# Optimization experiments

Hardware: AMD Instinct MI355X
Metric: run time of the kernel (lower is better)

Reference implementation:

```python
import jax, jax.numpy as jnp
import numpy as np

F = 50  # number of feature fields

def setup_inputs() -> dict:
    key = jax.random.key(0)
    k1, k2, k3, k4 = jax.random.split(key, 4)
    B, D, A = 4096, 16, 32
    return {
        "feat_emb": jax.random.normal(k1, (B, F, D), dtype=jnp.float32),
        "W": jax.random.normal(k2, (D, A), dtype=jnp.float32) * 0.1,
        "h": jax.random.normal(k3, (A,), dtype=jnp.float32),
        "p_vec": jax.random.normal(k4, (D,), dtype=jnp.float32),
    }

def reference(feat_emb, W, h, p_vec):
    # build_cross: upper-triangular field pairs (i < j)
    row, col = np.triu_indices(F, k=1)              # each [P], P = F*(F-1)/2
    p = feat_emb[:, row]                             # [B, P, D]
    q = feat_emb[:, col]                             # [B, P, D]
    inter = p * q                                    # pairwise interaction [B, P, D]
    # AttLayer: Dense(no bias) -> relu -> contract with h -> softmax over pairs
    att_signal = jax.nn.relu(jnp.einsum('bpd,da->bpa', inter, W))  # [B, P, A]
    scores = jnp.einsum('bpa,a->bp', att_signal, h)                # [B, P]
    att = jax.nn.softmax(scores, axis=1)                           # [B, P]
    # attention-weighted sum-pooling over pairs
    pooled = jnp.einsum('bp,bpd->bd', att, inter)                  # [B, D]
    # dropout omitted (inference); final projection and reduce
    out = jnp.einsum('bd,d->b', pooled, p_vec)[:, None]            # [B, 1]
    return out
```

## Files before the change

### kernel.cpp

```cpp
#include <hip/hip_runtime.h>
#include <math.h>


#define FF 50
#define DD 16
#define AA 32
#define NP 1225
#define NT 39
#define NQ4 10
#define ERS 24
#define EBS (FF * ERS)
#define BPB 8
#define NTHR 512

typedef _Float16 half8 __attribute__((ext_vector_type(8)));
typedef _Float16 half4 __attribute__((ext_vector_type(4)));
typedef _Float16 half2v __attribute__((ext_vector_type(2)));
typedef __fp16   fh2    __attribute__((ext_vector_type(2)));
typedef float    floatx16 __attribute__((ext_vector_type(16)));

__global__ __launch_bounds__(NTHR, 4) void afm_kernel(
    const float* __restrict__ feat,
    const float* __restrict__ W,
    const float* __restrict__ h,
    const float* __restrict__ pvec,
    float* __restrict__ out,
    int Btot)
{
  __shared__ __align__(16) _Float16 eh[BPB * EBS];
  __shared__ __align__(16) unsigned int tbl[NQ4 * 128];

  const int tid    = threadIdx.x;
  const int lane   = tid & 63;
  const int wave   = tid >> 6;
  const int halfid = lane >> 5;
  const int n      = lane & 31;
  const int b0     = blockIdx.x * BPB;

  for (int s = tid; s < BPB * 200; s += NTHR) {
    int bl  = s / 200;
    int rem = s - bl * 200;
    int bb  = b0 + bl;
    if (bb < Btot) {
      float4 v4 = ((const float4*)feat)[(size_t)bb * 200 + rem];
      half4 hv;
      hv[0] = (_Float16)v4.x; hv[1] = (_Float16)v4.y;
      hv[2] = (_Float16)v4.z; hv[3] = (_Float16)v4.w;
      int row = rem >> 2, q = rem & 3;
      *(half4*)(&eh[bl * EBS + row * ERS + q * 4]) = hv;
    }
  }

  for (int q = tid; q < NQ4 * 128; q += NTHR) {
    int q4  = q >> 7;
    int rem = q & 127;
    int nn  = rem >> 2;
    int u   = rem & 3;
    int p   = (4 * q4 + u) * 32 + nn;
    unsigned ent = 0;
    if (p < NP) {
      int rad = 9801 - 8 * p;
      int i = (int)((99.0f - sqrtf((float)rad)) * 0.5f);
      if (i < 0) i = 0; if (i > 48) i = 48;
      int off = (i * (99 - i)) >> 1;
      if (off > p) { --i; off = (i * (99 - i)) >> 1; }
      else {
        int off1 = ((i + 1) * (98 - i)) >> 1;
        if (off1 <= p) { ++i; off = off1; }
      }
      int j = p - off + i + 1;
      ent = ((unsigned)(i * 48) << 16) | (unsigned)(j * 48);
    }
    tbl[q] = ent;
  }

  const float LOG2E = 1.4426950408889634f;
  half8 A0;
  #pragma unroll
  for (int jj = 0; jj < 8; ++jj)
    A0[jj] = (_Float16)W[(halfid * 8 + jj) * AA + n];
  fh2 h2[8];
  #pragma unroll
  for (int q = 0; q < 8; ++q) {
    h2[q][0] = (__fp16)(h[((2*q) & 3) + 8 * ((2*q) >> 2) + 4 * halfid] * LOG2E);
    h2[q][1] = (__fp16)(h[((2*q+1) & 3) + 8 * ((2*q+1) >> 2) + 4 * halfid] * LOG2E);
  }
  fh2 pv2[4];
  #pragma unroll
  for (int q = 0; q < 4; ++q) {
    pv2[q][0] = (__fp16)pvec[halfid * 8 + 2 * q];
    pv2[q][1] = (__fp16)pvec[halfid * 8 + 2 * q + 1];
  }
  const floatx16 ZACC = (floatx16)0.0f;
  const fh2 zz = {(__fp16)0.f, (__fp16)0.f};

  __syncthreads();

  const char* eb = (const char*)(eh + wave * EBS) + halfid * 16;
  const unsigned int* tq = tbl + n * 4;

#if __has_builtin(__builtin_amdgcn_exp2f)
  #define EXP2(x) __builtin_amdgcn_exp2f(x)
#else
  #define EXP2(x) exp2f(x)
#endif

  auto mkB = [&](unsigned ij, float& gout) -> half8 {
    half8 Bi = *(const half8*)(eb + (ij >> 16));
    half8 Bj = *(const half8*)(eb + (ij & 0xffffu));
    half8 Bv = Bi * Bj;
#if __has_builtin(__builtin_amdgcn_fdot2)
    fh2 q0 = __builtin_bit_cast(fh2, (half2v)__builtin_shufflevector(Bv, Bv, 0, 1));
    fh2 q1 = __builtin_bit_cast(fh2, (half2v)__builtin_shufflevector(Bv, Bv, 2, 3));
    fh2 q2 = __builtin_bit_cast(fh2, (half2v)__builtin_shufflevector(Bv, Bv, 4, 5));
    fh2 q3 = __builtin_bit_cast(fh2, (half2v)__builtin_shufflevector(Bv, Bv, 6, 7));
    gout = __builtin_amdgcn_fdot2(q1, pv2[1],
           __builtin_amdgcn_fdot2(q0, pv2[0], 0.f, false), false)
         + __builtin_amdgcn_fdot2(q3, pv2[3],
           __builtin_amdgcn_fdot2(q2, pv2[2], 0.f, false), false);
#else
    float gp = 0.f;
    #pragma unroll
    for (int k = 0; k < 8; ++k)
      gp = fmaf((float)Bv[k], (float)((const __fp16*)pv2)[k], gp);
    gout = gp;
#endif
    return Bv;
  };
  auto epi = [&](const floatx16& z) -> float {
    float vL = 0.f, vH = 0.f;
    #pragma unroll
    for (int q = 0; q < 4; ++q) {
      fh2 zp = __builtin_amdgcn_cvt_pkrtz(z[2*q], z[2*q+1]);
      fh2 zr = __builtin_elementwise_max(zp, zz);
      vL = __builtin_amdgcn_fdot2(zr, h2[q], vL, false);
    }
    #pragma unroll
    for (int q = 4; q < 8; ++q) {
      fh2 zp = __builtin_amdgcn_cvt_pkrtz(z[2*q], z[2*q+1]);
      fh2 zr = __builtin_elementwise_max(zp, zz);
      vH = __builtin_amdgcn_fdot2(zr, h2[q], vH, false);
    }
    return vL + vH;
  };

  float den0 = 0.f, num0 = 0.f, den1 = 0.f, num1 = 0.f;

  for (int q4 = 0; q4 < 9; ++q4) {
    uint4 cur = *(const uint4*)(tq + (q4 << 7));
    float g0, g1, g2, g3;
    half8 B0 = mkB(cur.x, g0);
    half8 B1 = mkB(cur.y, g1);
    half8 B2 = mkB(cur.z, g2);
    half8 B3 = mkB(cur.w, g3);
    floatx16 z0 = __builtin_amdgcn_mfma_f32_32x32x16_f16(A0, B0, ZACC, 0, 0, 0);
    floatx16 z1 = __builtin_amdgcn_mfma_f32_32x32x16_f16(A0, B1, ZACC, 0, 0, 0);
    floatx16 z2 = __builtin_amdgcn_mfma_f32_32x32x16_f16(A0, B2, ZACC, 0, 0, 0);
    floatx16 z3 = __builtin_amdgcn_mfma_f32_32x32x16_f16(A0, B3, ZACC, 0, 0, 0);
    float p0 = epi(z0), p1 = epi(z1), p2 = epi(z2), p3 = epi(z3);
    float s0 = __shfl_xor(p0, 32, 64);
    float s1 = __shfl_xor(p1, 32, 64);
    float s2 = __shfl_xor(p2, 32, 64);
    float s3 = __shfl_xor(p3, 32, 64);
    float ex0 = EXP2(p0 + s0), ex1 = EXP2(p1 + s1);
    float ex2 = EXP2(p2 + s2), ex3 = EXP2(p3 + s3);
    den0 += ex0; num0 = fmaf(ex0, g0, num0);
    den1 += ex1; num1 = fmaf(ex1, g1, num1);
    den0 += ex2; num0 = fmaf(ex2, g2, num0);
    den1 += ex3; num1 = fmaf(ex3, g3, num1);
  }
  {
    uint4 cur = *(const uint4*)(tq + (9 << 7));
    float g0, g1, g2;
    half8 B0 = mkB(cur.x, g0);
    half8 B1 = mkB(cur.y, g1);
    half8 B2 = mkB(cur.z, g2);
    floatx16 z0 = __builtin_amdgcn_mfma_f32_32x32x16_f16(A0, B0, ZACC, 0, 0, 0);
    floatx16 z1 = __builtin_amdgcn_mfma_f32_32x32x16_f16(A0, B1, ZACC, 0, 0, 0);
    floatx16 z2 = __builtin_amdgcn_mfma_f32_32x32x16_f16(A0, B2, ZACC, 0, 0, 0);
    float p0 = epi(z0), p1 = epi(z1), p2 = epi(z2);
    float s0 = __shfl_xor(p0, 32, 64);
    float s1 = __shfl_xor(p1, 32, 64);
    float s2 = __shfl_xor(p2, 32, 64);
    float v2 = (n < 9) ? (p2 + s2) : -3.0e38f;
    float ex0 = EXP2(p0 + s0), ex1 = EXP2(p1 + s1), ex2 = EXP2(v2);
    den0 += ex0; num0 = fmaf(ex0, g0, num0);
    den1 += ex1; num1 = fmaf(ex1, g1, num1);
    den0 += ex2; num0 = fmaf(ex2, g2, num0);
  }
  float den = den0 + den1, num = num0 + num1;

  #pragma unroll
  for (int mask = 32; mask >= 1; mask >>= 1) {
    den += __shfl_xor(den, mask, 64);
    num += __shfl_xor(num, mask, 64);
  }
  const int b = b0 + wave;
  if (lane == 0 && b < Btot) out[b] = (2.0f * num) / den;
}

extern "C" void kernel_launch(void* const* d_in, const int* in_sizes, int n_in,
                              void* d_out, int out_size, void* d_ws, size_t ws_size,
                              hipStream_t stream) {
  const float* feat = (const float*)d_in[0];
  const float* W    = (const float*)d_in[1];
  const float* h    = (const float*)d_in[2];
  const float* pvec = (const float*)d_in[3];
  float* out = (float*)d_out;
  const int B = in_sizes[0] / (FF * DD);
  afm_kernel<<<(B + BPB - 1) / BPB, NTHR, 0, stream>>>(feat, W, h, pvec, out, B);
}
```

Baseline: 81.45 us.

## Move score and projection dot products from fdot2 into MFMA instructions

Replaces the per-lane fdot2 reductions for the attention score (h contraction) and the p_vec projection with extra MFMA instructions. The relu'd accumulator fragments are repacked as B operands and multiplied by h-filled and p_vec-filled A matrices. This removes the cross-half shuffles and the dot-product VALU work. The cost is three extra MFMAs per tile, where only one output row of each is used, so matrix-core throughput is largely wasted.

```diff
diff --git a/kernel.cpp b/kernel.cpp
--- a/kernel.cpp
+++ b/kernel.cpp
@@ -15,9 +15,9 @@
 
 typedef _Float16 half8 __attribute__((ext_vector_type(8)));
 typedef _Float16 half4 __attribute__((ext_vector_type(4)));
-typedef _Float16 half2v __attribute__((ext_vector_type(2)));
 typedef __fp16   fh2    __attribute__((ext_vector_type(2)));
 typedef float    floatx16 __attribute__((ext_vector_type(16)));
+typedef unsigned int uintv4 __attribute__((ext_vector_type(4)));
 
 __global__ __launch_bounds__(NTHR, 4) void afm_kernel(
     const float* __restrict__ feat,
@@ -79,17 +79,13 @@
   #pragma unroll
   for (int jj = 0; jj < 8; ++jj)
     A0[jj] = (_Float16)W[(halfid * 8 + jj) * AA + n];
-  fh2 h2[8];
+  half8 A2_0, A2_16, Apv;
   #pragma unroll
-  for (int q = 0; q < 8; ++q) {
-    h2[q][0] = (__fp16)(h[((2*q) & 3) + 8 * ((2*q) >> 2) + 4 * halfid] * LOG2E);
-    h2[q][1] = (__fp16)(h[((2*q+1) & 3) + 8 * ((2*q+1) >> 2) + 4 * halfid] * LOG2E);
-  }
-  fh2 pv2[4];
-  #pragma unroll
-  for (int q = 0; q < 4; ++q) {
-    pv2[q][0] = (__fp16)pvec[halfid * 8 + 2 * q];
-    pv2[q][1] = (__fp16)pvec[halfid * 8 + 2 * q + 1];
+  for (int jj = 0; jj < 8; ++jj) {
+    int arow = 4 * halfid + (jj & 3) + 8 * (jj >> 2);
+    A2_0[jj]  = (_Float16)(h[arow]      * LOG2E);
+    A2_16[jj] = (_Float16)(h[16 + arow] * LOG2E);
+    Apv[jj]   = (_Float16)pvec[halfid * 8 + jj];
   }
   const floatx16 ZACC = (floatx16)0.0f;
   const fh2 zz = {(__fp16)0.f, (__fp16)0.f};
@@ -105,88 +101,67 @@
   #define EXP2(x) exp2f(x)
 #endif
 
-  auto mkB = [&](unsigned ij, float& gout) -> half8 {
+  auto mkB = [&](unsigned ij) -> half8 {
     half8 Bi = *(const half8*)(eb + (ij >> 16));
     half8 Bj = *(const half8*)(eb + (ij & 0xffffu));
-    half8 Bv = Bi * Bj;
-#if __has_builtin(__builtin_amdgcn_fdot2)
-    fh2 q0 = __builtin_bit_cast(fh2, (half2v)__builtin_shufflevector(Bv, Bv, 0, 1));
-    fh2 q1 = __builtin_bit_cast(fh2, (half2v)__builtin_shufflevector(Bv, Bv, 2, 3));
-    fh2 q2 = __builtin_bit_cast(fh2, (half2v)__builtin_shufflevector(Bv, Bv, 4, 5));
-    fh2 q3 = __builtin_bit_cast(fh2, (half2v)__builtin_shufflevector(Bv, Bv, 6, 7));
-    gout = __builtin_amdgcn_fdot2(q1, pv2[1],
-           __builtin_amdgcn_fdot2(q0, pv2[0], 0.f, false), false)
-         + __builtin_amdgcn_fdot2(q3, pv2[3],
-           __builtin_amdgcn_fdot2(q2, pv2[2], 0.f, false), false);
-#else
-    float gp = 0.f;
+    return Bi * Bj;
+  };
+
+  auto score_frags = [&](const floatx16& z, half8& BL, half8& BH) {
+    unsigned q[8];
     #pragma unroll
-    for (int k = 0; k < 8; ++k)
-      gp = fmaf((float)Bv[k], (float)((const __fp16*)pv2)[k], gp);
-    gout = gp;
-#endif
-    return Bv;
-  };
-  auto epi = [&](const floatx16& z) -> float {
-    float vL = 0.f, vH = 0.f;
-    #pragma unroll
-    for (int q = 0; q < 4; ++q) {
-      fh2 zp = __builtin_amdgcn_cvt_pkrtz(z[2*q], z[2*q+1]);
+    for (int i = 0; i < 8; ++i) {
+      fh2 zp = __builtin_amdgcn_cvt_pkrtz(z[2 * i], z[2 * i + 1]);
       fh2 zr = __builtin_elementwise_max(zp, zz);
-      vL = __builtin_amdgcn_fdot2(zr, h2[q], vL, false);
+      q[i] = __builtin_bit_cast(unsigned, zr);
     }
-    #pragma unroll
-    for (int q = 4; q < 8; ++q) {
-      fh2 zp = __builtin_amdgcn_cvt_pkrtz(z[2*q], z[2*q+1]);
-      fh2 zr = __builtin_elementwise_max(zp, zz);
-      vH = __builtin_amdgcn_fdot2(zr, h2[q], vH, false);
-    }
-    return vL + vH;
+    uintv4 bl = {q[0], q[1], q[2], q[3]};
+    uintv4 bh = {q[4], q[5], q[6], q[7]};
+    BL = __builtin_bit_cast(half8, bl);
+    BH = __builtin_bit_cast(half8, bh);
   };
 
   float den0 = 0.f, num0 = 0.f, den1 = 0.f, num1 = 0.f;
 
+  auto tilepair = [&](unsigned ija, unsigned ijb) {
+    half8 Ba = mkB(ija);
+    half8 Bb = mkB(ijb);
+    floatx16 gA = __builtin_amdgcn_mfma_f32_32x32x16_f16(Apv, Ba, ZACC, 0, 0, 0);
+    floatx16 gB = __builtin_amdgcn_mfma_f32_32x32x16_f16(Apv, Bb, ZACC, 0, 0, 0);
+    floatx16 za = __builtin_amdgcn_mfma_f32_32x32x16_f16(A0, Ba, ZACC, 0, 0, 0);
+    floatx16 zb = __builtin_amdgcn_mfma_f32_32x32x16_f16(A0, Bb, ZACC, 0, 0, 0);
+    float ga = gA[0], gb = gB[0];
+    half8 BLa, BHa, BLb, BHb;
+    score_frags(za, BLa, BHa);
+    score_frags(zb, BLb, BHb);
+    floatx16 sa = __builtin_amdgcn_mfma_f32_32x32x16_f16(A2_0, BLa, ZACC, 0, 0, 0);
+    sa = __builtin_amdgcn_mfma_f32_32x32x16_f16(A2_16, BHa, sa, 0, 0, 0);
+    floatx16 sb = __builtin_amdgcn_mfma_f32_32x32x16_f16(A2_0, BLb, ZACC, 0, 0, 0);
+    sb = __builtin_amdgcn_mfma_f32_32x32x16_f16(A2_16, BHb, sb, 0, 0, 0);
+    float exa = EXP2(sa[0]);
+    float exb = EXP2(sb[0]);
+    den0 += exa; num0 = fmaf(exa, ga, num0);
+    den1 += exb; num1 = fmaf(exb, gb, num1);
+  };
+
   for (int q4 = 0; q4 < 9; ++q4) {
     uint4 cur = *(const uint4*)(tq + (q4 << 7));
-    float g0, g1, g2, g3;
-    half8 B0 = mkB(cur.x, g0);
-    half8 B1 = mkB(cur.y, g1);
-    half8 B2 = mkB(cur.z, g2);
-    half8 B3 = mkB(cur.w, g3);
-    floatx16 z0 = __builtin_amdgcn_mfma_f32_32x32x16_f16(A0, B0, ZACC, 0, 0, 0);
-    floatx16 z1 = __builtin_amdgcn_mfma_f32_32x32x16_f16(A0, B1, ZACC, 0, 0, 0);
-    floatx16 z2 = __builtin_amdgcn_mfma_f32_32x32x16_f16(A0, B2, ZACC, 0, 0, 0);
-    floatx16 z3 = __builtin_amdgcn_mfma_f32_32x32x16_f16(A0, B3, ZACC, 0, 0, 0);
-    float p0 = epi(z0), p1 = epi(z1), p2 = epi(z2), p3 = epi(z3);
-    float s0 = __shfl_xor(p0, 32, 64);
-    float s1 = __shfl_xor(p1, 32, 64);
-    float s2 = __shfl_xor(p2, 32, 64);
-    float s3 = __shfl_xor(p3, 32, 64);
-    float ex0 = EXP2(p0 + s0), ex1 = EXP2(p1 + s1);
-    float ex2 = EXP2(p2 + s2), ex3 = EXP2(p3 + s3);
-    den0 += ex0; num0 = fmaf(ex0, g0, num0);
-    den1 += ex1; num1 = fmaf(ex1, g1, num1);
-    den0 += ex2; num0 = fmaf(ex2, g2, num0);
-    den1 += ex3; num1 = fmaf(ex3, g3, num1);
+    tilepair(cur.x, cur.y);
+    tilepair(cur.z, cur.w);
   }
   {
     uint4 cur = *(const uint4*)(tq + (9 << 7));
-    float g0, g1, g2;
-    half8 B0 = mkB(cur.x, g0);
-    half8 B1 = mkB(cur.y, g1);
-    half8 B2 = mkB(cur.z, g2);
-    floatx16 z0 = __builtin_amdgcn_mfma_f32_32x32x16_f16(A0, B0, ZACC, 0, 0, 0);
-    floatx16 z1 = __builtin_amdgcn_mfma_f32_32x32x16_f16(A0, B1, ZACC, 0, 0, 0);
-    floatx16 z2 = __builtin_amdgcn_mfma_f32_32x32x16_f16(A0, B2, ZACC, 0, 0, 0);
-    float p0 = epi(z0), p1 = epi(z1), p2 = epi(z2);
-    float s0 = __shfl_xor(p0, 32, 64);
-    float s1 = __shfl_xor(p1, 32, 64);
-    float s2 = __shfl_xor(p2, 32, 64);
-    float v2 = (n < 9) ? (p2 + s2) : -3.0e38f;
-    float ex0 = EXP2(p0 + s0), ex1 = EXP2(p1 + s1), ex2 = EXP2(v2);
-    den0 += ex0; num0 = fmaf(ex0, g0, num0);
-    den1 += ex1; num1 = fmaf(ex1, g1, num1);
-    den0 += ex2; num0 = fmaf(ex2, g2, num0);
+    tilepair(cur.x, cur.y);
+    half8 Bc = mkB(cur.z);
+    floatx16 gC = __builtin_amdgcn_mfma_f32_32x32x16_f16(Apv, Bc, ZACC, 0, 0, 0);
+    floatx16 zc = __builtin_amdgcn_mfma_f32_32x32x16_f16(A0, Bc, ZACC, 0, 0, 0);
+    half8 BL, BH;
+    score_frags(zc, BL, BH);
+    floatx16 sc16 = __builtin_amdgcn_mfma_f32_32x32x16_f16(A2_0, BL, ZACC, 0, 0, 0);
+    sc16 = __builtin_amdgcn_mfma_f32_32x32x16_f16(A2_16, BH, sc16, 0, 0, 0);
+    float scv = (n < 9) ? sc16[0] : -3.0e38f;
+    float exc = EXP2(scv);
+    den0 += exc; num0 = fmaf(exc, gC[0], num0);
   }
   float den = den0 + den1, num = num0 + num1;
 
@@ -196,7 +171,7 @@
     num += __shfl_xor(num, mask, 64);
   }
   const int b = b0 + wave;
-  if (lane == 0 && b < Btot) out[b] = (2.0f * num) / den;
+  if (lane == 0 && b < Btot) out[b] = num / den;
 }
 
 extern "C" void kernel_launch(void* const* d_in, const int* in_sizes, int n_in,
```

New measurement: 81.26 us. Within noise of the previous version (-0.2%).
